# Kernel optimization log

Hardware: AMD Instinct MI355X
Metric: run time of the kernel (lower is better)

The kernel has to match this reference:

```python
import jax, jax.numpy as jnp
import numpy as np

N_ANCH = 100800   # 3 * (160^2 + 80^2 + 40^2), YOLOv5 @ 1280
NUM_CLS = 80
IMG_HW = 1280
MAX_DETS = 300    # fixed padding for jit-compatible NMS output
OUT = 224
SCORE_THRESH = 0.1
IOU_THRESH = 0.45
ALLOWED = jnp.array([1, 2, 3, 4, 6, 8, 17, 18, 44], dtype=jnp.int32)
MEAN = jnp.array([0.485, 0.456, 0.406], dtype=jnp.float32).reshape(1, 3, 1, 1)
STD = jnp.array([0.229, 0.224, 0.225], dtype=jnp.float32).reshape(1, 3, 1, 1)


def setup_inputs() -> dict:
    key = jax.random.key(0)
    k1, k2, k3, k4, k5 = jax.random.split(key, 5)
    # realistic YOLO-style raw predictions: cx,cy in-image, modest w,h, gaussian class logits
    cxcy = jax.random.uniform(k1, (1, 2, N_ANCH), dtype=jnp.float32) * IMG_HW
    wh = jax.random.uniform(k2, (1, 2, N_ANCH), dtype=jnp.float32) * 256.0 + 8.0
    obj = jax.random.uniform(k3, (1, 1, N_ANCH), dtype=jnp.float32)
    logits = jax.random.normal(k4, (1, NUM_CLS, N_ANCH), dtype=jnp.float32)
    raw_pred = jnp.concatenate([cxcy, wh, obj, logits], axis=1)  # [1, 5+C, N]
    image = jax.random.uniform(k5, (1, 3, IMG_HW, IMG_HW), dtype=jnp.float32)
    return {"raw_pred": raw_pred, "image": image}


def _pairwise_iou(b):
    # b: [K,4] xyxy
    area = (b[:, 2] - b[:, 0]) * (b[:, 3] - b[:, 1])
    lt = jnp.maximum(b[:, None, :2], b[None, :, :2])
    rb = jnp.minimum(b[:, None, 2:], b[None, :, 2:])
    wh = jnp.clip(rb - lt, 0.0)
    inter = wh[..., 0] * wh[..., 1]
    union = area[:, None] + area[None, :] - inter
    return inter / jnp.maximum(union, 1e-9)


def _nms_keep(iou, valid):
    # greedy NMS over score-sorted boxes; returns boolean keep mask [K]
    K = iou.shape[0]
    idx = jnp.arange(K)

    def body(i, keep):
        suppress = keep[i] & (iou[i] > IOU_THRESH) & (idx > i)
        return keep & ~suppress

    return jax.lax.fori_loop(0, K, body, valid)


def _roi_align(image_chw, boxes):
    # torchvision roi_align, aligned=True, one sample per bin at the bin center
    # (sampling_ratio fixed to 1; see notes). image_chw: [3,H,W], boxes: [M,4]
    C, H, W = image_chw.shape
    grid = (jnp.arange(OUT, dtype=jnp.float32) + 0.5) / OUT  # fractional bin centers

    def one(box):
        x1, y1, x2, y2 = box
        xs = x1 - 0.5 + grid * (x2 - x1)  # [OUT], aligned=True half-pixel offset
        ys = y1 - 0.5 + grid * (y2 - y1)
        vx = (xs >= -1.0) & (xs <= W)
        vy = (ys >= -1.0) & (ys <= H)
        xc = jnp.clip(xs, 0.0, W - 1)
        yc = jnp.clip(ys, 0.0, H - 1)
        x0 = jnp.floor(xc).astype(jnp.int32)
        y0 = jnp.floor(yc).astype(jnp.int32)
        x1i = jnp.minimum(x0 + 1, W - 1)
        y1i = jnp.minimum(y0 + 1, H - 1)
        lx = xc - x0
        ly = yc - y0
        # bilinear gather: [3, OUT, OUT]
        v00 = image_chw[:, y0[:, None], x0[None, :]]
        v01 = image_chw[:, y0[:, None], x1i[None, :]]
        v10 = image_chw[:, y1i[:, None], x0[None, :]]
        v11 = image_chw[:, y1i[:, None], x1i[None, :]]
        top = v00 * (1.0 - lx) + v01 * lx
        bot = v10 * (1.0 - lx) + v11 * lx
        val = top * (1.0 - ly)[None, :, None] + bot * ly[None, :, None]
        return jnp.where(vy[None, :, None] & vx[None, None, :], val, 0.0)

    return jax.vmap(one)(boxes)


def _forward(raw_pred, image):
    x = raw_pred[0].T  # [N, 5+C]
    cx, cy, w, h = x[:, 0], x[:, 1], x[:, 2], x[:, 3]
    boxes = jnp.stack([cx - w / 2, cy - h / 2, cx + w / 2, cy + h / 2], axis=1)
    cls_logits = x[:, 5:]
    scores = cls_logits.max(axis=1)
    classes = cls_logits.argmax(axis=1).astype(jnp.int32) + 1
    # score + allowed-class filter (mask form)
    mask = (scores > SCORE_THRESH) & jnp.isin(classes, ALLOWED)
    masked_scores = jnp.where(mask, scores, jnp.finfo(scores.dtype).min)
    top_scores, top_idx = jax.lax.top_k(masked_scores, MAX_DETS)  # sorted desc
    top_boxes = boxes[top_idx]
    top_classes = classes[top_idx]
    valid = mask[top_idx]
    # greedy NMS over padded top-K candidates
    keep = _nms_keep(_pairwise_iou(top_boxes), valid)
    final_boxes = jnp.where(keep[:, None], top_boxes, 0.0)
    final_scores = jnp.where(keep, top_scores, 0.0)
    final_classes = jnp.where(keep, top_classes, 0)
    # crops: full image first, then RoIAlign crops, normalized once
    full_crop = jax.image.resize(image, (1, 3, OUT, OUT), method='linear', antialias=False)
    roi_crops = _roi_align(image[0], final_boxes)  # [K,3,224,224]
    roi_crops = jnp.where(keep[:, None, None, None], roi_crops, 0.0)
    all_crops = jnp.concatenate([full_crop, roi_crops], axis=0)  # [K+1,3,224,224]
    all_crops = (all_crops - MEAN) / STD
    return final_boxes, final_scores, final_classes, all_crops, keep


def reference(raw_pred, image):
    return _forward(raw_pred, image)
```

## Files before the change

### kernel.cpp

```cpp
#include <hip/hip_runtime.h>
#include <stdint.h>

#define N_ANCH   100800
#define NUM_CLS  80
#define IMG_HW   1280
#define MAX_DETS 300
#define OUTSZ    224
#define CAND_CAP 4096

#define OFF_BOXES   0
#define OFF_SCORES  1200
#define OFF_CLASSES 1500
#define OFF_CROPS   1800
#define CROPS_ELEMS (301 * 3 * 224 * 224)
#define OFF_KEEP    (OFF_CROPS + CROPS_ELEMS)

#define SC_HIST   0
#define SC_CNT    262144
#define SC_THRESH 262148
#define SC_CAND   262208
#define SC_KEYS   294976
#define SC_CLS    698176

typedef float f32x4 __attribute__((ext_vector_type(4)));

__device__ __forceinline__ uint32_t fkey(float f) {
    uint32_t u = __float_as_uint(f);
    return (u & 0x80000000u) ? ~u : (u | 0x80000000u);
}
__device__ __forceinline__ float unfkey(uint32_t k) {
    uint32_t u = (k & 0x80000000u) ? (k & 0x7fffffffu) : ~k;
    return __uint_as_float(u);
}

__global__ void k_score(const float* __restrict__ rp, uint32_t* __restrict__ keys,
                        uint32_t* __restrict__ hist, uint32_t* __restrict__ clsarr) {
    int a4 = (blockIdx.x * 256 + threadIdx.x) * 4;
    if (a4 >= N_ANCH) return;
    float best[4] = {-3.402823466e38f, -3.402823466e38f, -3.402823466e38f, -3.402823466e38f};
    int bi[4] = {0, 0, 0, 0};
    for (int c = 0; c < NUM_CLS; ++c) {
        float4 v = *(const float4*)&rp[(5 + c) * N_ANCH + a4];
        if (v.x > best[0]) { best[0] = v.x; bi[0] = c; }
        if (v.y > best[1]) { best[1] = v.y; bi[1] = c; }
        if (v.z > best[2]) { best[2] = v.z; bi[2] = c; }
        if (v.w > best[3]) { best[3] = v.w; bi[3] = c; }
    }
    const unsigned long long AM =
        (1ULL << 1) | (1ULL << 2) | (1ULL << 3) | (1ULL << 4) | (1ULL << 6) |
        (1ULL << 8) | (1ULL << 17) | (1ULL << 18) | (1ULL << 44);
    uint32_t kv[4], cv[4];
    #pragma unroll
    for (int k = 0; k < 4; ++k) {
        int cls = bi[k] + 1;
        cv[k] = (uint32_t)cls;
        bool m = (best[k] > 0.1f) && (cls < 64) && ((AM >> cls) & 1ULL);
        kv[k] = m ? fkey(best[k]) : 0u;
    }
    *(uint4*)&keys[a4]   = make_uint4(kv[0], kv[1], kv[2], kv[3]);
    *(uint4*)&clsarr[a4] = make_uint4(cv[0], cv[1], cv[2], cv[3]);
    #pragma unroll
    for (int k = 0; k < 4; ++k)
        if (kv[k]) atomicAdd(&hist[kv[k] >> 16], 1u);
}

__global__ void k_scan(const uint32_t* __restrict__ hist, uint32_t* __restrict__ thresh_out) {
    __shared__ uint32_t seg[256];
    int t = threadIdx.x;
    uint32_t s = 0;
    for (int k = 0; k < 256; ++k) s += hist[t * 256 + k];
    seg[t] = s;
    __syncthreads();
    if (t == 0) {
        uint32_t acc = 0;
        int bin = 0, sIdx = -1;
        for (int i = 255; i >= 0; --i) {
            if (acc + seg[i] >= (uint32_t)MAX_DETS) { sIdx = i; break; }
            acc += seg[i];
        }
        if (sIdx >= 0) {
            for (int b = sIdx * 256 + 255; b >= sIdx * 256; --b) {
                acc += hist[b];
                if (acc >= (uint32_t)MAX_DETS) { bin = b; break; }
            }
        }
        *thresh_out = (uint32_t)bin;
    }
}

__global__ void k_compact(const uint32_t* __restrict__ keys, const uint32_t* __restrict__ thresh_p,
                          unsigned long long* __restrict__ cand, uint32_t* __restrict__ cnt) {
    int a4 = (blockIdx.x * 256 + threadIdx.x) * 4;
    if (a4 >= N_ANCH) return;
    uint4 kv = *(const uint4*)&keys[a4];
    uint32_t tb = *thresh_p;
    uint32_t ks[4] = {kv.x, kv.y, kv.z, kv.w};
    #pragma unroll
    for (int k = 0; k < 4; ++k) {
        uint32_t key = ks[k];
        if (key != 0u && (key >> 16) >= tb) {
            uint32_t pos = atomicAdd(cnt, 1u);
            if (pos < CAND_CAP) {
                uint32_t a = (uint32_t)(a4 + k);
                cand[pos] = ((unsigned long long)key << 32) | (uint32_t)(~a);
            }
        }
    }
}

__global__ void __launch_bounds__(1024) k_select(const float* __restrict__ rp,
                                                 const uint32_t* __restrict__ clsarr,
                                                 const unsigned long long* __restrict__ cand,
                                                 const uint32_t* __restrict__ cnt_p,
                                                 float* __restrict__ out) {
    __shared__ unsigned long long sb[CAND_CAP];
    __shared__ unsigned long long top[MAX_DETS];
    __shared__ float sbx[MAX_DETS][4];
    __shared__ float sscore[MAX_DETS];
    __shared__ int   scls[MAX_DETS];
    __shared__ __align__(8) uint32_t sup[MAX_DETS][10];
    __shared__ __align__(8) uint32_t kw[10];
    __shared__ __align__(8) uint32_t rnz[10];
    int t = threadIdx.x;
    int n = min((int)(*cnt_p), CAND_CAP);

    for (int i = t; i < n; i += 1024) sb[i] = cand[i];
    if (t < MAX_DETS) top[t] = 0ull;
    __syncthreads();

    for (int i = t; i < n; i += 1024) {
        unsigned long long key = sb[i];
        int rank = 0;
        for (int j = 0; j < n; ++j) rank += (sb[j] > key) ? 1 : 0;
        if (rank < MAX_DETS) top[rank] = key;
    }
    __syncthreads();

    for (int i = t; i < MAX_DETS * 10; i += 1024) ((uint32_t*)sup)[i] = 0u;
    if (t < 10) { kw[t] = 0u; rnz[t] = 0u; }
    __syncthreads();

    if (t < MAX_DETS) {
        unsigned long long key = top[t];
        bool valid = (key != 0ull);
        float score = 0.f; int cls = 0;
        float b0 = 0.f, b1 = 0.f, b2 = 0.f, b3 = 0.f;
        if (valid) {
            uint32_t a = ~(uint32_t)(key & 0xffffffffull);
            score = unfkey((uint32_t)(key >> 32));
            float cx = rp[a], cy = rp[N_ANCH + a];
            float w = rp[2 * N_ANCH + a], h = rp[3 * N_ANCH + a];
            b0 = cx - w * 0.5f; b1 = cy - h * 0.5f;
            b2 = cx + w * 0.5f; b3 = cy + h * 0.5f;
            cls = (int)clsarr[a];
            atomicOr(&kw[t >> 5], 1u << (t & 31));
        }
        sbx[t][0] = b0; sbx[t][1] = b1; sbx[t][2] = b2; sbx[t][3] = b3;
        sscore[t] = score; scls[t] = cls;
    }
    __syncthreads();

    for (int p = t; p < MAX_DETS * MAX_DETS; p += 1024) {
        int i = p / MAX_DETS, j = p % MAX_DETS;
        if (j > i) {
            float ax1 = sbx[i][0], ay1 = sbx[i][1], ax2 = sbx[i][2], ay2 = sbx[i][3];
            float bx1 = sbx[j][0], by1 = sbx[j][1], bx2 = sbx[j][2], by2 = sbx[j][3];
            float areaA = (ax2 - ax1) * (ay2 - ay1);
            float areaB = (bx2 - bx1) * (by2 - by1);
            float ltx = fmaxf(ax1, bx1), lty = fmaxf(ay1, by1);
            float rbx = fminf(ax2, bx2), rby = fminf(ay2, by2);
            float iw = fmaxf(rbx - ltx, 0.f), ih = fmaxf(rby - lty, 0.f);
            float inter = iw * ih;
            float uni = areaA + areaB - inter;
            float iou = inter / fmaxf(uni, 1e-9f);
            if (iou > 0.45f) {
                atomicOr(&sup[i][j >> 5], 1u << (j & 31));
                atomicOr(&rnz[i >> 5], 1u << (i & 31));
            }
        }
    }
    __syncthreads();

    if (t == 0) {
        unsigned long long kwr[5], rnzr[5];
        const unsigned long long* kq = (const unsigned long long*)kw;
        const unsigned long long* rq = (const unsigned long long*)rnz;
        #pragma unroll
        for (int w = 0; w < 5; ++w) { kwr[w] = kq[w]; rnzr[w] = rq[w]; }
        #pragma unroll
        for (int s = 0; s < 5; ++s) {
            int lim = (s == 4) ? (MAX_DETS - 4 * 64) : 64;
            for (int i2 = 0; i2 < lim; ++i2) {
                if (((kwr[s] >> i2) & 1ull) && ((rnzr[s] >> i2) & 1ull)) {
                    int i = s * 64 + i2;
                    const unsigned long long* row = (const unsigned long long*)&sup[i][0];
                    unsigned long long r0 = row[0], r1 = row[1], r2 = row[2],
                                       r3 = row[3], r4 = row[4];
                    kwr[0] &= ~r0; kwr[1] &= ~r1; kwr[2] &= ~r2;
                    kwr[3] &= ~r3; kwr[4] &= ~r4;
                }
            }
        }
        unsigned long long* kqo = (unsigned long long*)kw;
        #pragma unroll
        for (int w = 0; w < 5; ++w) kqo[w] = kwr[w];
    }
    __syncthreads();

    if (t < MAX_DETS) {
        bool kp = (kw[t >> 5] >> (t & 31)) & 1u;
        out[OFF_BOXES + t * 4 + 0] = kp ? sbx[t][0] : 0.f;
        out[OFF_BOXES + t * 4 + 1] = kp ? sbx[t][1] : 0.f;
        out[OFF_BOXES + t * 4 + 2] = kp ? sbx[t][2] : 0.f;
        out[OFF_BOXES + t * 4 + 3] = kp ? sbx[t][3] : 0.f;
        out[OFF_SCORES + t]  = kp ? sscore[t] : 0.f;
        out[OFF_CLASSES + t] = kp ? (float)scls[t] : 0.f;
        out[OFF_KEEP + t]    = kp ? 1.f : 0.f;
    }
}

__device__ __forceinline__ float bilerp(const float* __restrict__ ch, float xc, float yc) {
    int x0 = (int)floorf(xc), y0 = (int)floorf(yc);
    int x1 = min(x0 + 1, IMG_HW - 1), y1 = min(y0 + 1, IMG_HW - 1);
    float lx = xc - (float)x0, ly = yc - (float)y0;
    float v00 = ch[y0 * IMG_HW + x0], v01 = ch[y0 * IMG_HW + x1];
    float v10 = ch[y1 * IMG_HW + x0], v11 = ch[y1 * IMG_HW + x1];
    return (v00 * (1.f - lx) + v01 * lx) * (1.f - ly) +
           (v10 * (1.f - lx) + v11 * lx) * ly;
}

__global__ void k_crops(const float* __restrict__ img, float* __restrict__ out) {
    int nc = blockIdx.y;
    int n = nc / 3, c = nc % 3;
    int q = blockIdx.x * 256 + threadIdx.x;
    int oy = q / (OUTSZ / 4);
    int ox0 = (q % (OUTSZ / 4)) * 4;
    const float meanv[3] = {0.485f, 0.456f, 0.406f};
    const float stdv[3]  = {0.229f, 0.224f, 0.225f};
    float mean = meanv[c], rstd = 1.0f / stdv[c];
    const float* ch = img + c * IMG_HW * IMG_HW;
    f32x4 v;
    if (n == 0) {
        float sy = ((float)oy + 0.5f) * (1280.0f / 224.0f) - 0.5f;
        #pragma unroll
        for (int k = 0; k < 4; ++k) {
            float sx = ((float)(ox0 + k) + 0.5f) * (1280.0f / 224.0f) - 0.5f;
            v[k] = (bilerp(ch, sx, sy) - mean) * rstd;
        }
    } else {
        float kp = out[OFF_KEEP + (n - 1)];
        if (kp == 0.f) {
            float z = (0.f - mean) * rstd;
            v = (f32x4){z, z, z, z};
        } else {
            float x1b = out[OFF_BOXES + (n - 1) * 4 + 0];
            float y1b = out[OFF_BOXES + (n - 1) * 4 + 1];
            float x2b = out[OFF_BOXES + (n - 1) * 4 + 2];
            float y2b = out[OFF_BOXES + (n - 1) * 4 + 3];
            float gy = ((float)oy + 0.5f) / 224.0f;
            float ys = y1b - 0.5f + gy * (y2b - y1b);
            bool vy = (ys >= -1.0f) && (ys <= 1280.0f);
            float yc = fminf(fmaxf(ys, 0.f), 1279.f);
            #pragma unroll
            for (int k = 0; k < 4; ++k) {
                float gx = ((float)(ox0 + k) + 0.5f) / 224.0f;
                float xs = x1b - 0.5f + gx * (x2b - x1b);
                bool vx = (xs >= -1.0f) && (xs <= 1280.0f);
                float xc = fminf(fmaxf(xs, 0.f), 1279.f);
                float val = bilerp(ch, xc, yc);
                if (!(vx && vy)) val = 0.f;
                v[k] = (val - mean) * rstd;
            }
        }
    }
    f32x4* dst = (f32x4*)(out + OFF_CROPS + (size_t)nc * (OUTSZ * OUTSZ) + oy * OUTSZ + ox0);
    __builtin_nontemporal_store(v, dst);
}

extern "C" void kernel_launch(void* const* d_in, const int* in_sizes, int n_in,
                              void* d_out, int out_size, void* d_ws, size_t ws_size,
                              hipStream_t stream) {
    (void)in_sizes; (void)n_in; (void)out_size; (void)d_ws; (void)ws_size;
    const float* rp  = (const float*)d_in[0];
    const float* img = (const float*)d_in[1];
    float* out = (float*)d_out;
    char* sbase = (char*)d_out + (size_t)OFF_CROPS * sizeof(float);
    uint32_t* hist = (uint32_t*)(sbase + SC_HIST);
    uint32_t* cnt  = (uint32_t*)(sbase + SC_CNT);
    uint32_t* thr  = (uint32_t*)(sbase + SC_THRESH);
    unsigned long long* cand = (unsigned long long*)(sbase + SC_CAND);
    uint32_t* keys = (uint32_t*)(sbase + SC_KEYS);
    uint32_t* clsa = (uint32_t*)(sbase + SC_CLS);

    hipMemsetAsync(sbase, 0, SC_CAND, stream);
    k_score<<<(N_ANCH / 4 + 255) / 256, 256, 0, stream>>>(rp, keys, hist, clsa);
    k_scan<<<1, 256, 0, stream>>>(hist, thr);
    k_compact<<<(N_ANCH / 4 + 255) / 256, 256, 0, stream>>>(keys, thr, cand, cnt);
    k_select<<<1, 1024, 0, stream>>>(rp, clsa, cand, cnt, out);
    dim3 grid(49, 903);
    k_crops<<<grid, 256, 0, stream>>>(img, out);
}
```

Before: 371.4 us.

## Split class argmax across lanes, parallelize histogram scan, XCD-aware crop block mapping

```diff
diff --git a/kernel.cpp b/kernel.cpp
--- a/kernel.cpp
+++ b/kernel.cpp
@@ -35,27 +35,44 @@
 
 __global__ void k_score(const float* __restrict__ rp, uint32_t* __restrict__ keys,
                         uint32_t* __restrict__ hist, uint32_t* __restrict__ clsarr) {
-    int a4 = (blockIdx.x * 256 + threadIdx.x) * 4;
-    if (a4 >= N_ANCH) return;
+    int gid = blockIdx.x * 256 + threadIdx.x;
+    int grp = gid >> 3;
+    int cp  = gid & 7;
+    if (grp >= N_ANCH / 4) return;
+    int a4 = grp * 4;
+
     float best[4] = {-3.402823466e38f, -3.402823466e38f, -3.402823466e38f, -3.402823466e38f};
-    int bi[4] = {0, 0, 0, 0};
-    for (int c = 0; c < NUM_CLS; ++c) {
-        float4 v = *(const float4*)&rp[(5 + c) * N_ANCH + a4];
-        if (v.x > best[0]) { best[0] = v.x; bi[0] = c; }
-        if (v.y > best[1]) { best[1] = v.y; bi[1] = c; }
-        if (v.z > best[2]) { best[2] = v.z; bi[2] = c; }
-        if (v.w > best[3]) { best[3] = v.w; bi[3] = c; }
-    }
+    int   bc[4]   = {0, 0, 0, 0};
+    #pragma unroll
+    for (int k = 0; k < 10; ++k) {
+        int c = cp + 8 * k;
+        float4 v = *(const float4*)&rp[(size_t)(5 + c) * N_ANCH + a4];
+        if (v.x > best[0]) { best[0] = v.x; bc[0] = c; }
+        if (v.y > best[1]) { best[1] = v.y; bc[1] = c; }
+        if (v.z > best[2]) { best[2] = v.z; bc[2] = c; }
+        if (v.w > best[3]) { best[3] = v.w; bc[3] = c; }
+    }
+    #pragma unroll
+    for (int m = 1; m < 8; m <<= 1) {
+        #pragma unroll
+        for (int j = 0; j < 4; ++j) {
+            float ob = __shfl_xor(best[j], m);
+            int   oc = __shfl_xor(bc[j], m);
+            if (ob > best[j] || (ob == best[j] && oc < bc[j])) { best[j] = ob; bc[j] = oc; }
+        }
+    }
+    if (cp != 0) return;
+
     const unsigned long long AM =
         (1ULL << 1) | (1ULL << 2) | (1ULL << 3) | (1ULL << 4) | (1ULL << 6) |
         (1ULL << 8) | (1ULL << 17) | (1ULL << 18) | (1ULL << 44);
     uint32_t kv[4], cv[4];
     #pragma unroll
     for (int k = 0; k < 4; ++k) {
-        int cls = bi[k] + 1;
+        int cls = bc[k] + 1;
         cv[k] = (uint32_t)cls;
-        bool m = (best[k] > 0.1f) && (cls < 64) && ((AM >> cls) & 1ULL);
-        kv[k] = m ? fkey(best[k]) : 0u;
+        bool mk = (best[k] > 0.1f) && (cls < 64) && ((AM >> cls) & 1ULL);
+        kv[k] = mk ? fkey(best[k]) : 0u;
     }
     *(uint4*)&keys[a4]   = make_uint4(kv[0], kv[1], kv[2], kv[3]);
     *(uint4*)&clsarr[a4] = make_uint4(cv[0], cv[1], cv[2], cv[3]);
@@ -64,25 +81,52 @@
         if (kv[k]) atomicAdd(&hist[kv[k] >> 16], 1u);
 }
 
-__global__ void k_scan(const uint32_t* __restrict__ hist, uint32_t* __restrict__ thresh_out) {
-    __shared__ uint32_t seg[256];
+__global__ void __launch_bounds__(1024) k_scan(const uint32_t* __restrict__ hist,
+                                               uint32_t* __restrict__ thresh_out) {
+    __shared__ uint32_t ssum[1024];
+    __shared__ uint32_t swave[16];
+    __shared__ int      sh_ssel;
+    __shared__ uint32_t sh_acc;
+    __shared__ uint32_t sbin[64];
     int t = threadIdx.x;
+    const uint4* h4 = (const uint4*)(hist + t * 64);
     uint32_t s = 0;
-    for (int k = 0; k < 256; ++k) s += hist[t * 256 + k];
-    seg[t] = s;
+    #pragma unroll
+    for (int i = 0; i < 16; ++i) { uint4 v = h4[i]; s += v.x + v.y + v.z + v.w; }
+    ssum[t] = s;
+    uint32_t ws = s;
+    #pragma unroll
+    for (int m = 32; m; m >>= 1) ws += __shfl_xor(ws, m);
+    if ((t & 63) == 0) swave[t >> 6] = ws;
     __syncthreads();
     if (t == 0) {
-        uint32_t acc = 0;
-        int bin = 0, sIdx = -1;
-        for (int i = 255; i >= 0; --i) {
-            if (acc + seg[i] >= (uint32_t)MAX_DETS) { sIdx = i; break; }
-            acc += seg[i];
-        }
-        if (sIdx >= 0) {
-            for (int b = sIdx * 256 + 255; b >= sIdx * 256; --b) {
-                acc += hist[b];
-                if (acc >= (uint32_t)MAX_DETS) { bin = b; break; }
-            }
+        uint32_t acc = 0; int wsel = -1;
+        for (int w = 15; w >= 0; --w) {
+            uint32_t v = swave[w];
+            if (acc + v >= (uint32_t)MAX_DETS) { wsel = w; break; }
+            acc += v;
+        }
+        int ssel = -1;
+        if (wsel >= 0) {
+            for (int sg = wsel * 64 + 63; sg >= wsel * 64; --sg) {
+                uint32_t v = ssum[sg];
+                if (acc + v >= (uint32_t)MAX_DETS) { ssel = sg; break; }
+                acc += v;
+            }
+        }
+        sh_ssel = ssel; sh_acc = acc;
+    }
+    __syncthreads();
+    int ssel = sh_ssel;
+    if (ssel < 0) { if (t == 0) *thresh_out = 0u; return; }
+    if (t < 64) sbin[t] = hist[ssel * 64 + t];
+    __syncthreads();
+    if (t == 0) {
+        uint32_t acc = sh_acc;
+        int bin = 0;
+        for (int b = 63; b >= 0; --b) {
+            acc += sbin[b];
+            if (acc >= (uint32_t)MAX_DETS) { bin = ssel * 64 + b; break; }
         }
         *thresh_out = (uint32_t)bin;
     }
@@ -219,6 +263,9 @@
     }
 }
 
+#define BLKS_PER_CROP 147
+#define SLOTS_PER_XCD (38 * BLKS_PER_CROP)
+
 __device__ __forceinline__ float bilerp(const float* __restrict__ ch, float xc, float yc) {
     int x0 = (int)floorf(xc), y0 = (int)floorf(yc);
     int x1 = min(x0 + 1, IMG_HW - 1), y1 = min(y0 + 1, IMG_HW - 1);
@@ -230,9 +277,16 @@
 }
 
 __global__ void k_crops(const float* __restrict__ img, float* __restrict__ out) {
-    int nc = blockIdx.y;
-    int n = nc / 3, c = nc % 3;
-    int q = blockIdx.x * 256 + threadIdx.x;
+    int bid  = blockIdx.x;
+    int xcd  = bid & 7;
+    int slot = bid >> 3;
+    int n = xcd + 8 * (slot / BLKS_PER_CROP);
+    if (n > 300) return;
+    int inner = slot % BLKS_PER_CROP;
+    int c  = inner / 49;
+    int bx = inner % 49;
+    int nc = n * 3 + c;
+    int q = bx * 256 + threadIdx.x;
     int oy = q / (OUTSZ / 4);
     int ox0 = (q % (OUTSZ / 4)) * 4;
     const float meanv[3] = {0.485f, 0.456f, 0.406f};
@@ -293,10 +347,9 @@
     uint32_t* clsa = (uint32_t*)(sbase + SC_CLS);
 
     hipMemsetAsync(sbase, 0, SC_CAND, stream);
-    k_score<<<(N_ANCH / 4 + 255) / 256, 256, 0, stream>>>(rp, keys, hist, clsa);
-    k_scan<<<1, 256, 0, stream>>>(hist, thr);
+    k_score<<<(N_ANCH / 4 * 8 + 255) / 256, 256, 0, stream>>>(rp, keys, hist, clsa);
+    k_scan<<<1, 1024, 0, stream>>>(hist, thr);
     k_compact<<<(N_ANCH / 4 + 255) / 256, 256, 0, stream>>>(keys, thr, cand, cnt);
     k_select<<<1, 1024, 0, stream>>>(rp, clsa, cand, cnt, out);
-    dim3 grid(49, 903);
-    k_crops<<<grid, 256, 0, stream>>>(img, out);
-}
+    k_crops<<<8 * SLOTS_PER_XCD, 256, 0, stream>>>(img, out);
+}
```

New measurement: 382.7 us. 3.0% more time.
